# Optimization experiments

Hardware: AMD Instinct MI355X
Metric: run time of the kernel (lower is better)

The kernel has to match this reference:

```python
import jax, jax.numpy as jnp
import numpy as np

H = 1024          # hidden_size
M = 512           # moe_intermediate_size
E = 16            # num_routed_experts
TOP_K = 2         # num_experts_per_tok
SCALE = 2.5       # routed_scaling_factor
NORM_TOPK = True  # norm_topk_prob
B, S = 1, 1024


def setup_inputs() -> dict:
    key = jax.random.key(0)
    ks = jax.random.split(key, 8)
    std = 0.02
    return {
        "hidden_states": jax.random.normal(ks[0], (B, S, H), jnp.float32),
        "gate_w": jax.random.normal(ks[1], (E, H), jnp.float32) * std,
        "w_gate": jax.random.normal(ks[2], (E, H, M), jnp.float32) * std,
        "w_up": jax.random.normal(ks[3], (E, H, M), jnp.float32) * std,
        "w_down": jax.random.normal(ks[4], (E, M, H), jnp.float32) * std,
        "ws_gate": jax.random.normal(ks[5], (H, M), jnp.float32) * std,
        "ws_up": jax.random.normal(ks[6], (H, M), jnp.float32) * std,
        "ws_down": jax.random.normal(ks[7], (M, H), jnp.float32) * std,
    }


def _moe(x, gate_w, w_gate, w_up, w_down, ws_gate, ws_up, ws_down):
    # x: [T, H] flattened tokens
    T = x.shape[0]
    # shared expert (SwiGLU): down(silu(gate(x)) * up(x))
    shared = (jax.nn.silu(x @ ws_gate) * (x @ ws_up)) @ ws_down  # [T, H]

    # sigmoid gating in fp32 (matches F.linear on fp32 + sigmoid)
    scores = jax.nn.sigmoid(x.astype(jnp.float32) @ gate_w.T.astype(jnp.float32))  # [T, E]
    topk_w, topk_idx = jax.lax.top_k(scores, TOP_K)  # [T, K]
    if NORM_TOPK and TOP_K > 1:
        topk_w = topk_w / (topk_w.sum(-1, keepdims=True) + 1e-20)
    topk_w = topk_w * SCALE

    # dense combine weights [T, E]; zero for non-selected experts, so weighting
    # all-expert outputs is mathematically identical to the dispatch/gather path
    route = jnp.zeros((T, E), topk_w.dtype).at[jnp.arange(T)[:, None], topk_idx].set(topk_w)

    # per-expert SwiGLU over all tokens (grouped-GEMM reference)
    g = jnp.einsum("th,ehm->etm", x, w_gate)                 # [E, T, M]
    u = jnp.einsum("th,ehm->etm", x, w_up)                   # [E, T, M]
    eo = jnp.einsum("etm,emh->eth", jax.nn.silu(g) * u, w_down)  # [E, T, H]
    routed = jnp.einsum("te,eth->th", route.astype(x.dtype), eo)  # [T, H]
    return routed + shared


def reference(hidden_states, gate_w, w_gate, w_up, w_down, ws_gate, ws_up, ws_down):
    b, s, h = hidden_states.shape
    x = hidden_states.reshape(-1, h)
    out = _moe(x, gate_w, w_gate, w_up, w_down, ws_gate, ws_up, ws_down)
    return out.reshape(b, s, h)
```

## Files before the change

kernel.cpp:

```cpp
#include <hip/hip_runtime.h>
#include <math.h>

#define TT 1024
#define HH 1024
#define MM 512
#define NE 16

typedef _Float16 f16;
typedef _Float16 f16x4 __attribute__((ext_vector_type(4)));
typedef _Float16 f16x8 __attribute__((ext_vector_type(8)));
typedef float f32x4 __attribute__((ext_vector_type(4)));

#define GLL(g, l) __builtin_amdgcn_global_load_lds(                         \
    (const __attribute__((address_space(1))) void*)(g),                     \
    (__attribute__((address_space(3))) void*)(l), 16, 0, 0)
#define SB() __builtin_amdgcn_sched_barrier(0)
#define WAITVM(N) { SB(); asm volatile("s_waitcnt vmcnt(" #N ")"); SB(); }
#define BARRIER() __builtin_amdgcn_s_barrier()

__global__ __launch_bounds__(256) void pack_k(const float* __restrict__ x, f16* __restrict__ xh)
{
    const int i = (blockIdx.x * 256 + threadIdx.x) * 4;
    float4 v = *(const float4*)(x + i);
    f16x4 h = { (f16)v.x, (f16)v.y, (f16)v.z, (f16)v.w };
    *(f16x4*)(xh + i) = h;
}

__global__ __launch_bounds__(256) void router_k(
    const float* __restrict__ x, const float* __restrict__ gate_w,
    int* __restrict__ counts, int* __restrict__ token_list, float* __restrict__ weight_list)
{
    const int wave = threadIdx.x >> 6;
    const int lane = threadIdx.x & 63;
    const int t = (blockIdx.x << 2) + wave;
    const float* xr = x + (size_t)t * HH;
    float xv[16];
#pragma unroll
    for (int i = 0; i < 16; ++i) xv[i] = xr[lane + (i << 6)];
    float sc[NE];
#pragma unroll
    for (int e = 0; e < NE; ++e) {
        const float* gr = gate_w + e * HH;
        float acc = 0.f;
#pragma unroll
        for (int i = 0; i < 16; ++i) acc = fmaf(xv[i], gr[lane + (i << 6)], acc);
#pragma unroll
        for (int off = 32; off > 0; off >>= 1) acc += __shfl_down(acc, off, 64);
        sc[e] = acc;
    }
    if (lane == 0) {
        float l1 = -1e30f, l2 = -1e30f; int i1 = 0, i2 = 0;
#pragma unroll
        for (int e = 0; e < NE; ++e) {
            float v = sc[e];
            if (v > l1) { l2 = l1; i2 = i1; l1 = v; i1 = e; }
            else if (v > l2) { l2 = v; i2 = e; }
        }
        float w1 = 1.f / (1.f + __expf(-l1));
        float w2 = 1.f / (1.f + __expf(-l2));
        const float inv = 2.5f / (w1 + w2 + 1e-20f);
        w1 *= inv; w2 *= inv;
        int s1 = atomicAdd(&counts[i1], 1);
        token_list[i1 * TT + s1] = t;
        weight_list[i1 * TT + s1] = w1;
        int s2 = atomicAdd(&counts[i2], 1);
        token_list[i2 * TT + s2] = t;
        weight_list[i2 * TT + s2] = w2;
    }
}

__global__ void prefix_k(const int* __restrict__ counts, int* __restrict__ offs)
{
    if (threadIdx.x == 0 && blockIdx.x == 0) {
        int acc = 0;
#pragma unroll
        for (int e = 0; e < NE; ++e) { offs[e] = acc; acc += counts[e]; }
        offs[NE] = acc;
    }
}


#define GU_ISSUE(T2, AS, BG, BU) {                                          \
    _Pragma("unroll") for (int i = 0; i < 2; ++i) {                         \
        GLL(pA[i] + ((T2) << 6), &AS[(w << 4) + (i << 3)][0]);              \
        GLL(pBg[i] + (size_t)((T2) << 6) * MM, &BG[(w << 4) + (i << 3)][0]);\
        GLL(pBu[i] + (size_t)((T2) << 6) * MM, &BU[(w << 4) + (i << 3)][0]); } }

#define GU_COMP(AS, BG, BU) {                                               \
    _Pragma("unroll") for (int h = 0; h < 2; ++h) {                         \
        const int kb = (h << 5) + (lg << 3);                                \
        const int ko = (h << 2) + lg;                                       \
        f16x8 af[2];                                                        \
        _Pragma("unroll") for (int f = 0; f < 2; ++f) {                     \
            const int m = wm + (f << 4) + lm;                               \
            af[f] = *(const f16x8*)&AS[m][(ko ^ (m & 7)) << 3];             \
        }                                                                   \
        const int bc = (wn + lm) ^ ((lg & 1) << 4);                         \
        f16x8 bg, bu;                                                       \
        _Pragma("unroll") for (int j = 0; j < 8; ++j) {                     \
            bg[j] = (f16)BG[kb + j][bc]; bu[j] = (f16)BU[kb + j][bc]; }     \
        _Pragma("unroll") for (int f = 0; f < 2; ++f) {                     \
            accg[f] = __builtin_amdgcn_mfma_f32_16x16x32_f16(af[f], bg, accg[f], 0, 0, 0); \
            accu[f] = __builtin_amdgcn_mfma_f32_16x16x32_f16(af[f], bu, accu[f], 0, 0, 0); } } }

#define GU_PHI(T2, AI, BC, VC) { GU_ISSUE(T2, As##AI, Bg##AI, Bu##AI)       \
    WAITVM(VC) BARRIER();                                                   \
    GU_COMP(As##BC, Bg##BC, Bu##BC) BARRIER(); }
#define GU_PHN(BC, VC) { WAITVM(VC) BARRIER();                              \
    GU_COMP(As##BC, Bg##BC, Bu##BC) BARRIER(); }

__global__ __launch_bounds__(256) void gu_k(
    const f16* __restrict__ xh,
    const float* __restrict__ w_gate, const float* __restrict__ w_up,
    const float* __restrict__ ws_gate, const float* __restrict__ ws_up,
    const int* __restrict__ counts, const int* __restrict__ offs,
    const int* __restrict__ token_list, f16* __restrict__ rinter)
{
    const int F = blockIdx.x;
    const int Q = F & 7;
    const int J = F >> 3;
    int e, tile;
    if (J < 512) { e = Q + ((J >> 8) << 3); tile = J & 255; }
    else         { e = NE; tile = (Q << 5) + (J - 512); }
    const int n0 = (tile & 15) << 5;
    const int r0 = (tile >> 4) << 6;

    int cnt, slot0;
    const float *wgp, *wup;
    if (e < NE) {
        cnt = counts[e]; slot0 = offs[e];
        wgp = w_gate + (size_t)e * HH * MM;
        wup = w_up   + (size_t)e * HH * MM;
    } else {
        cnt = TT; slot0 = 2 * TT;
        wgp = ws_gate; wup = ws_up;
    }
    if (r0 >= cnt) return;

    __shared__ f16  As0[64][64], As1[64][64], As2[64][64];
    __shared__ float Bg0[64][32], Bg1[64][32], Bg2[64][32];
    __shared__ float Bu0[64][32], Bu1[64][32], Bu2[64][32];
    __shared__ int toks[64];

    const int tid = threadIdx.x;
    if (tid < 64) {
        int i = r0 + tid; if (i >= cnt) i = cnt - 1;
        toks[tid] = (e < NE) ? token_list[e * TT + i] : i;
    }
    __syncthreads();

    const int w = tid >> 6, lane = tid & 63;
    const int lm = lane & 15, lg = lane >> 4;
    const int wm = (w >> 1) << 5, wn = (w & 1) << 4;

    const f16* pA[2];
#pragma unroll
    for (int i = 0; i < 2; ++i) {
        int m = (w << 4) + (i << 3) + (lane >> 3);
        pA[i] = xh + (size_t)toks[m] * HH + (((lane & 7) ^ (lane >> 3)) << 3);
    }
    const float* pBg[2]; const float* pBu[2];
#pragma unroll
    for (int i = 0; i < 2; ++i) {
        int kr = (w << 4) + (i << 3) + (lane >> 3);
        int sg = 4 * ((lane & 7) ^ ((i & 1) << 2));
        pBg[i] = wgp + (size_t)kr * MM + n0 + sg;
        pBu[i] = wup + (size_t)kr * MM + n0 + sg;
    }

    f32x4 accg[2] = {}, accu[2] = {};

    GU_ISSUE(0, As0, Bg0, Bu0)
    GU_ISSUE(1, As1, Bg1, Bu1)

    GU_PHI(2,2,0,12)  GU_PHI(3,0,1,12)  GU_PHI(4,1,2,12)  GU_PHI(5,2,0,12)
    GU_PHI(6,0,1,12)  GU_PHI(7,1,2,12)  GU_PHI(8,2,0,12)  GU_PHI(9,0,1,12)
    GU_PHI(10,1,2,12) GU_PHI(11,2,0,12) GU_PHI(12,0,1,12) GU_PHI(13,1,2,12)
    GU_PHI(14,2,0,12) GU_PHI(15,0,1,12)
    GU_PHN(2,6)       GU_PHN(0,0)

#pragma unroll
    for (int fi = 0; fi < 2; ++fi)
#pragma unroll
        for (int rr = 0; rr < 4; ++rr) {
            const int m = wm + (fi << 4) + (lg << 2) + rr;
            if (r0 + m < cnt) {
                float g = (fi ? accg[1] : accg[0])[rr];
                float u = (fi ? accu[1] : accu[0])[rr];
                float s = g / (1.f + __expf(-g));
                rinter[(size_t)(slot0 + r0 + m) * MM + n0 + wn + lm] = (f16)(s * u);
            }
        }
}


#define DN_ISSUE(T, AS, BS) {                                               \
    GLL(pa0 + ((T) << 5), &AS[w << 5][0]);                                  \
    GLL(pa1 + ((T) << 5), &AS[(w << 5) + 16][0]);                           \
    GLL(pb0 + (size_t)((T) << 5) * HH, &BS[w << 3][0]);                     \
    GLL(pb1 + (size_t)((T) << 5) * HH, &BS[(w << 3) + 4][0]); }

#define DN_COMP(AS, BS) {                                                   \
    f16x8 af[2];                                                            \
    _Pragma("unroll") for (int f = 0; f < 2; ++f) {                         \
        const int m = (w << 5) + (f << 4) + lm;                             \
        af[f] = *(const f16x8*)&AS[m][(lg ^ ((m >> 1) & 3)) << 3];          \
    }                                                                       \
    _Pragma("unroll") for (int nf = 0; nf < 4; ++nf) {                      \
        const int bc = ((nf << 4) + lm) ^ ((lg & 1) << 4);                  \
        f16x8 bv;                                                           \
        _Pragma("unroll") for (int j = 0; j < 8; ++j) bv[j] = (f16)BS[(lg << 3) + j][bc]; \
        _Pragma("unroll") for (int f = 0; f < 2; ++f)                       \
            acc[f][nf] = __builtin_amdgcn_mfma_f32_16x16x32_f16(af[f], bv, acc[f][nf], 0, 0, 0); } }

#define DN_PH(T, CB, IB, VC) {                                              \
    if ((T) + 2 < 16) DN_ISSUE((T) + 2, As##IB, Bs##IB)                     \
    WAITVM(VC) BARRIER();                                                   \
    DN_COMP(As##CB, Bs##CB)                                                 \
    BARRIER(); }

__global__ __launch_bounds__(256) void down_k(
    const f16* __restrict__ rinter,
    const float* __restrict__ w_down, const float* __restrict__ ws_down,
    const int* __restrict__ counts, const int* __restrict__ offs,
    const int* __restrict__ token_list, const float* __restrict__ weight_list,
    float* __restrict__ out)
{
    const int F = blockIdx.x;
    const int Q = F & 7;
    const int J = F >> 3;
    int e, n0, r0;
    if (J < 256) {
        e = Q + ((J >> 7) << 3);
        const int t = J & 127;
        n0 = (t & 15) << 6;
        r0 = (t >> 4) << 7;
    } else {
        e = NE;
        const int idx = (Q << 4) + (J - 256);
        n0 = (idx & 15) << 6;
        r0 = (idx >> 4) << 7;
    }

    int cnt, slot0; const float* wdp;
    if (e < NE) { cnt = counts[e]; slot0 = offs[e]; wdp = w_down + (size_t)e * MM * HH; }
    else        { cnt = TT; slot0 = 2 * TT; wdp = ws_down; }
    if (r0 >= cnt) return;

    __shared__ f16  As0[128][32], As1[128][32], As2[128][32];
    __shared__ float Bs0[32][64], Bs1[32][64], Bs2[32][64];

    const int tid = threadIdx.x;
    const int w = tid >> 6, lane = tid & 63;
    const int lm = lane & 15, lg = lane >> 4;

    const int swzA = ((lane & 3) ^ ((lane >> 3) & 3)) << 3;
    int ra = r0 + (w << 5) + (lane >> 2);       if (ra >= cnt) ra = cnt - 1;
    int rb = r0 + (w << 5) + 16 + (lane >> 2);  if (rb >= cnt) rb = cnt - 1;
    const f16* pa0 = rinter + (size_t)(slot0 + ra) * MM + swzA;
    const f16* pa1 = rinter + (size_t)(slot0 + rb) * MM + swzA;
    const int sgd = 4 * ((lane & 15) ^ ((w & 1) << 2));
    const float* pb0 = wdp + (size_t)((w << 3)     + (lane >> 4)) * HH + n0 + sgd;
    const float* pb1 = wdp + (size_t)((w << 3) + 4 + (lane >> 4)) * HH + n0 + sgd;

    f32x4 acc[2][4] = {};

    DN_ISSUE(0, As0, Bs0)
    DN_ISSUE(1, As1, Bs1)

    DN_PH(0,0,2,8)  DN_PH(1,1,0,8)  DN_PH(2,2,1,8)  DN_PH(3,0,2,8)
    DN_PH(4,1,0,8)  DN_PH(5,2,1,8)  DN_PH(6,0,2,8)  DN_PH(7,1,0,8)
    DN_PH(8,2,1,8)  DN_PH(9,0,2,8)  DN_PH(10,1,0,8) DN_PH(11,2,1,8)
    DN_PH(12,0,2,8) DN_PH(13,1,0,8) DN_PH(14,2,1,4) DN_PH(15,0,0,0)

#pragma unroll
    for (int f = 0; f < 2; ++f)
#pragma unroll
        for (int rr = 0; rr < 4; ++rr) {
            const int m = (w << 5) + (f << 4) + (lg << 2) + rr;
            const int row = r0 + m;
            if (row < cnt) {
                int t; float wt;
                if (e < NE) { t = token_list[e * TT + row]; wt = weight_list[e * TT + row]; }
                else        { t = row; wt = 1.f; }
                float* orow = out + (size_t)t * HH + n0;
#pragma unroll
                for (int nf = 0; nf < 4; ++nf)
                    atomicAdd(&orow[(nf << 4) + lm], wt * acc[f][nf][rr]);
            }
        }
}

extern "C" void kernel_launch(void* const* d_in, const int* in_sizes, int n_in,
                              void* d_out, int out_size, void* d_ws, size_t ws_size,
                              hipStream_t stream)
{
    const float* x       = (const float*)d_in[0];
    const float* gate_w  = (const float*)d_in[1];
    const float* w_gate  = (const float*)d_in[2];
    const float* w_up    = (const float*)d_in[3];
    const float* w_down  = (const float*)d_in[4];
    const float* ws_gate = (const float*)d_in[5];
    const float* ws_up   = (const float*)d_in[6];
    const float* ws_down = (const float*)d_in[7];
    float* out = (float*)d_out;

    int* counts = (int*)d_ws;
    int* offs = counts + 16;
    int* token_list = counts + 64;
    float* weight_list = (float*)(counts + 64 + NE * TT);
    f16* rinter = (f16*)(counts + 64 + 2 * NE * TT);
    f16* xh = rinter + (size_t)3072 * MM;

    hipMemsetAsync(counts, 0, 64, stream);
    hipMemsetAsync(out, 0, (size_t)TT * HH * sizeof(float), stream);
    pack_k<<<dim3(TT * HH / 1024), 256, 0, stream>>>(x, xh);
    router_k<<<dim3(TT / 4), 256, 0, stream>>>(x, gate_w, counts, token_list, weight_list);
    prefix_k<<<1, 64, 0, stream>>>(counts, offs);
    gu_k<<<dim3(8 * 544), 256, 0, stream>>>(
        xh, w_gate, w_up, ws_gate, ws_up, counts, offs, token_list, rinter);
    down_k<<<dim3(8 * 272), 256, 0, stream>>>(
        rinter, w_down, ws_down, counts, offs, token_list, weight_list, out);
}
```

Baseline: 99.83 us.

## Replace atomic output accumulation with per-slot fp16 partials and reduce kernel

The fp32-to-fp16 pack is fused into the router, which removes the pack kernel. The output memset and fp32 atomicAdd scatter are dropped. The shared expert now writes the output directly, and each routed expert writes a weighted fp16 partial into one of two buffers chosen by top-k slot. A new reduce kernel adds the two partials into the output. This avoids atomic contention and the memset, but adds an extra pass over memory and rounds the routed contributions to fp16.

```diff
diff --git a/kernel.cpp b/kernel.cpp
--- a/kernel.cpp
+++ b/kernel.cpp
@@ -18,17 +18,11 @@
 #define WAITVM(N) { SB(); asm volatile("s_waitcnt vmcnt(" #N ")"); SB(); }
 #define BARRIER() __builtin_amdgcn_s_barrier()
 
-__global__ __launch_bounds__(256) void pack_k(const float* __restrict__ x, f16* __restrict__ xh)
-{
-    const int i = (blockIdx.x * 256 + threadIdx.x) * 4;
-    float4 v = *(const float4*)(x + i);
-    f16x4 h = { (f16)v.x, (f16)v.y, (f16)v.z, (f16)v.w };
-    *(f16x4*)(xh + i) = h;
-}
-
 __global__ __launch_bounds__(256) void router_k(
     const float* __restrict__ x, const float* __restrict__ gate_w,
-    int* __restrict__ counts, int* __restrict__ token_list, float* __restrict__ weight_list)
+    int* __restrict__ counts, int* __restrict__ token_list,
+    float* __restrict__ weight_list, int* __restrict__ flag_list,
+    f16* __restrict__ xh)
 {
     const int wave = threadIdx.x >> 6;
     const int lane = threadIdx.x & 63;
@@ -37,6 +31,8 @@
     float xv[16];
 #pragma unroll
     for (int i = 0; i < 16; ++i) xv[i] = xr[lane + (i << 6)];
+#pragma unroll
+    for (int i = 0; i < 16; ++i) xh[(size_t)t * HH + lane + (i << 6)] = (f16)xv[i];
     float sc[NE];
 #pragma unroll
     for (int e = 0; e < NE; ++e) {
@@ -63,9 +59,11 @@
         int s1 = atomicAdd(&counts[i1], 1);
         token_list[i1 * TT + s1] = t;
         weight_list[i1 * TT + s1] = w1;
+        flag_list[i1 * TT + s1] = 0;
         int s2 = atomicAdd(&counts[i2], 1);
         token_list[i2 * TT + s2] = t;
         weight_list[i2 * TT + s2] = w2;
+        flag_list[i2 * TT + s2] = 1;
     }
 }
 
@@ -224,7 +222,8 @@
     const float* __restrict__ w_down, const float* __restrict__ ws_down,
     const int* __restrict__ counts, const int* __restrict__ offs,
     const int* __restrict__ token_list, const float* __restrict__ weight_list,
-    float* __restrict__ out)
+    const int* __restrict__ flag_list,
+    f16* __restrict__ pR0, f16* __restrict__ pR1, float* __restrict__ out)
 {
     const int F = blockIdx.x;
     const int Q = F & 7;
@@ -280,15 +279,41 @@
             const int m = (w << 5) + (f << 4) + (lg << 2) + rr;
             const int row = r0 + m;
             if (row < cnt) {
-                int t; float wt;
-                if (e < NE) { t = token_list[e * TT + row]; wt = weight_list[e * TT + row]; }
-                else        { t = row; wt = 1.f; }
-                float* orow = out + (size_t)t * HH + n0;
-#pragma unroll
-                for (int nf = 0; nf < 4; ++nf)
-                    atomicAdd(&orow[(nf << 4) + lm], wt * acc[f][nf][rr]);
+                if (e < NE) {
+                    const int t = token_list[e * TT + row];
+                    const float wt = weight_list[e * TT + row];
+                    f16* orow = (flag_list[e * TT + row] ? pR1 : pR0) + (size_t)t * HH + n0;
+#pragma unroll
+                    for (int nf = 0; nf < 4; ++nf)
+                        orow[(nf << 4) + lm] = (f16)(wt * acc[f][nf][rr]);
+                } else {
+                    float* orow = out + (size_t)row * HH + n0;
+#pragma unroll
+                    for (int nf = 0; nf < 4; ++nf)
+                        orow[(nf << 4) + lm] = acc[f][nf][rr];
+                }
             }
         }
+}
+
+__global__ __launch_bounds__(256) void reduce_k(
+    const f16* __restrict__ pR0, const f16* __restrict__ pR1, float* __restrict__ out)
+{
+    const int i = (blockIdx.x * 256 + threadIdx.x) * 8;
+    f16x8 a = *(const f16x8*)(pR0 + i);
+    f16x8 b = *(const f16x8*)(pR1 + i);
+    float4 o0 = *(const float4*)(out + i);
+    float4 o1 = *(const float4*)(out + i + 4);
+    o0.x += (float)a[0] + (float)b[0];
+    o0.y += (float)a[1] + (float)b[1];
+    o0.z += (float)a[2] + (float)b[2];
+    o0.w += (float)a[3] + (float)b[3];
+    o1.x += (float)a[4] + (float)b[4];
+    o1.y += (float)a[5] + (float)b[5];
+    o1.z += (float)a[6] + (float)b[6];
+    o1.w += (float)a[7] + (float)b[7];
+    *(float4*)(out + i) = o0;
+    *(float4*)(out + i + 4) = o1;
 }
 
 extern "C" void kernel_launch(void* const* d_in, const int* in_sizes, int n_in,
@@ -308,17 +333,21 @@
     int* counts = (int*)d_ws;
     int* offs = counts + 16;
     int* token_list = counts + 64;
-    float* weight_list = (float*)(counts + 64 + NE * TT);
-    f16* rinter = (f16*)(counts + 64 + 2 * NE * TT);
+    float* weight_list = (float*)(token_list + NE * TT);
+    int* flag_list = (int*)(weight_list + NE * TT);
+    f16* rinter = (f16*)(flag_list + NE * TT);
     f16* xh = rinter + (size_t)3072 * MM;
+    f16* pR0 = xh + (size_t)TT * HH;
+    f16* pR1 = pR0 + (size_t)TT * HH;
 
     hipMemsetAsync(counts, 0, 64, stream);
-    hipMemsetAsync(out, 0, (size_t)TT * HH * sizeof(float), stream);
-    pack_k<<<dim3(TT * HH / 1024), 256, 0, stream>>>(x, xh);
-    router_k<<<dim3(TT / 4), 256, 0, stream>>>(x, gate_w, counts, token_list, weight_list);
+    router_k<<<dim3(TT / 4), 256, 0, stream>>>(
+        x, gate_w, counts, token_list, weight_list, flag_list, xh);
     prefix_k<<<1, 64, 0, stream>>>(counts, offs);
     gu_k<<<dim3(8 * 544), 256, 0, stream>>>(
         xh, w_gate, w_up, ws_gate, ws_up, counts, offs, token_list, rinter);
     down_k<<<dim3(8 * 272), 256, 0, stream>>>(
-        rinter, w_down, ws_down, counts, offs, token_list, weight_list, out);
-}
+        rinter, w_down, ws_down, counts, offs, token_list, weight_list, flag_list,
+        pR0, pR1, out);
+    reduce_k<<<dim3(TT * HH / 2048), 256, 0, stream>>>(pR0, pR1, out);
+}
```

Result: faster. 94.00 us (-5.8%).
